# Kernel optimization log

Hardware: AMD Instinct MI355X
Metric: run time of the kernel (lower is better)

Reference implementation:

```python
import jax, jax.numpy as jnp
import numpy as np

N = 25000      # nodes
E = 400000     # edges (before self-loops)
F_IN = 128     # num_node_features
HID = 16       # hidden_channels
HEADS = 12     # GAT heads
OUT = 32       # output_channels


def setup_inputs() -> dict:
    key = jax.random.key(0)
    ks = jax.random.split(key, 16)
    def glorot(k, shape):
        fan_in = shape[0]
        return jax.random.normal(k, shape, jnp.float32) / np.sqrt(fan_in)
    return {
        "x": jax.random.normal(ks[0], (N, 1, F_IN), jnp.float32),
        "edge_index": jax.random.randint(ks[1], (2, E), 0, N, jnp.int64),
        # GCNConv 1
        "W1": glorot(ks[2], (F_IN, HID)),
        "b1": jnp.zeros((HID,), jnp.float32),
        # GATConv (heads=12, concat)
        "Wg": glorot(ks[3], (HID, HEADS * HID)),
        "att_src": jax.random.normal(ks[4], (HEADS, HID), jnp.float32) * 0.1,
        "att_dst": jax.random.normal(ks[5], (HEADS, HID), jnp.float32) * 0.1,
        "bg": jnp.zeros((HEADS * HID,), jnp.float32),
        # GCNConv 2 and 3
        "W2": glorot(ks[6], (HEADS * HID, HID)),
        "b2": jnp.zeros((HID,), jnp.float32),
        "W3": glorot(ks[7], (HID, HID)),
        "b3": jnp.zeros((HID,), jnp.float32),
        # final Linear
        "Wlin": glorot(ks[8], (HID, OUT)),
        "blin": jnp.zeros((OUT,), jnp.float32),
    }


def _add_self_loops(edge_index, n):
    loop = jnp.arange(n, dtype=edge_index.dtype)
    src = jnp.concatenate([edge_index[0], loop])
    dst = jnp.concatenate([edge_index[1], loop])
    return src, dst


def _gcn_conv(x, W, b, src, dst, n):
    # PyG GCNConv: symmetric normalization with self-loops (already in src/dst)
    h = x @ W                                            # [N, C]
    deg = jax.ops.segment_sum(jnp.ones_like(dst, jnp.float32), dst, n)
    dinv = jnp.where(deg > 0, jax.lax.rsqrt(deg), 0.0)   # deg^-0.5
    norm = dinv[src] * dinv[dst]                         # [E']
    out = jax.ops.segment_sum(h[src] * norm[:, None], dst, n)
    return out + b


def _gat_conv(x, Wg, att_src, att_dst, bg, src, dst, n):
    # PyG GATConv, concat=True, negative_slope=0.2, self-loops in src/dst
    h = (x @ Wg).reshape(n, HEADS, HID)                  # [N, H, C]
    a_s = jnp.sum(h * att_src, axis=-1)                  # [N, H]
    a_d = jnp.sum(h * att_dst, axis=-1)                  # [N, H]
    e = a_s[src] + a_d[dst]                              # [E', H]
    e = jnp.where(e > 0, e, 0.2 * e)                     # leaky_relu
    m = jax.ops.segment_max(e, dst, n)                   # stable softmax per dst
    ex = jnp.exp(e - m[dst])
    denom = jax.ops.segment_sum(ex, dst, n)
    alpha = ex / denom[dst]                              # [E', H]
    out = jax.ops.segment_sum(alpha[:, :, None] * h[src], dst, n)  # [N, H, C]
    return out.reshape(n, HEADS * HID) + bg


def reference(x, edge_index, W1, b1, Wg, att_src, att_dst, bg, W2, b2, W3, b3, Wlin, blin):
    n = x.shape[0]
    src, dst = _add_self_loops(edge_index, n)
    xs = x.squeeze(1)                                    # [N, F]
    x1 = jax.nn.relu(_gcn_conv(xs, W1, b1, src, dst, n))
    # dropout p=0.5 is identity in eval mode
    x2 = jax.nn.elu(_gat_conv(x1, Wg, att_src, att_dst, bg, src, dst, n))
    x3 = jax.nn.relu(_gcn_conv(x2, W2, b2, src, dst, n))
    x4 = jax.nn.relu(_gcn_conv(x3, W3, b3, src, dst, n)) + x3
    x4 = jnp.mean(x4, axis=0, keepdims=True)             # [1, HID]
    return x4 @ Wlin + blin                              # [1, OUT]
```

## Files before the change

kernel.cpp:

```cpp
#include <hip/hip_runtime.h>

#define F_IN 128
#define HID 16
#define HEADS 12
#define HF (HEADS*HID)
#define OUT_C 32

typedef _Float16 f16;

__global__ void k_detect(const int* __restrict__ ei, int E, int* __restrict__ flag) {
    __shared__ int sacc[256];
    int t = threadIdx.x;
    long long half = (long long)E;
    int acc = 0;
    #pragma unroll
    for (int i = 0; i < 8; i++) {
        long long k = ((long long)(t + i * 256) * half) / 2048;
        acc |= ei[2 * k + 1];
    }
    sacc[t] = acc;
    __syncthreads();
    for (int off = 128; off >= 1; off >>= 1) {
        if (t < off) sacc[t] |= sacc[t + off];
        __syncthreads();
    }
    if (t == 0) flag[1] = sacc[0];
}

__global__ void k_convert(const void* __restrict__ ei, int E, const int* __restrict__ flag,
                          int* __restrict__ src32, int* __restrict__ dst32,
                          int* __restrict__ count) {
    int e = blockIdx.x * blockDim.x + threadIdx.x;
    if (e >= E) return;
    int s, d;
    if (flag[1] == 0) {
        const long long* p = (const long long*)ei;
        s = (int)p[e];
        d = (int)p[(size_t)E + e];
    } else {
        const int* p = (const int*)ei;
        s = p[e];
        d = p[(size_t)E + e];
    }
    src32[e] = s;
    dst32[e] = d;
    atomicAdd(&count[d], 1);
}


__global__ void k_scan(const int* __restrict__ count, int* __restrict__ rowstart,
                       float* __restrict__ dinv, int n) {
    __shared__ int part[1024];
    int t = threadIdx.x;
    int chunk = (n + 1023) >> 10;
    int beg = t * chunk;
    int end = beg + chunk; if (end > n) end = n;
    int s = 0;
    for (int i = beg; i < end; i++) s += count[i];
    part[t] = s;
    __syncthreads();
    for (int off = 1; off < 1024; off <<= 1) {
        int v = (t >= off) ? part[t - off] : 0;
        __syncthreads();
        part[t] += v;
        __syncthreads();
    }
    int run = (t == 0) ? 0 : part[t - 1];
    for (int i = beg; i < end; i++) {
        rowstart[i] = run;
        int c = count[i];
        run += c;
        dinv[i] = rsqrtf((float)(c + 1));
    }
    if (t == 1023) rowstart[n] = run;
}

__global__ void k_fill(const int* __restrict__ srcA, const int* __restrict__ dstA, int E,
                       const int* __restrict__ rowstart, int* __restrict__ cursor,
                       int* __restrict__ csr) {
    int e = blockIdx.x * blockDim.x + threadIdx.x;
    if (e < E) {
        int d = dstA[e];
        int p = atomicAdd(&cursor[d], 1);
        csr[rowstart[d] + p] = srcA[e];
    }
}


__global__ void k_gemm1(const float* __restrict__ x, const float* __restrict__ W,
                        f16* __restrict__ h, int n) {
    __shared__ float sW[F_IN * HID];
    __shared__ float sX[16][F_IN + 1];
    int t = threadIdx.x;
    for (int i = t; i < F_IN * HID; i += 256) sW[i] = W[i];
    int node0 = blockIdx.x * 16;
    for (int i = t; i < 16 * F_IN; i += 256) {
        int r = i >> 7, c = i & 127;
        int node = node0 + r;
        sX[r][c] = (node < n) ? x[node * F_IN + c] : 0.f;
    }
    __syncthreads();
    int ln = t >> 4, c = t & 15;
    float acc = 0.f;
    #pragma unroll 8
    for (int k = 0; k < F_IN; k++) acc += sX[ln][k] * sW[k * HID + c];
    int node = node0 + ln;
    if (node < n) h[node * HID + c] = (f16)acc;
}

__global__ void k_gemm_gat(const float* __restrict__ x1, const float* __restrict__ Wg,
                           const float* __restrict__ att_s, const float* __restrict__ att_d,
                           f16* __restrict__ hg, float* __restrict__ a_s,
                           float* __restrict__ a_d, int n) {
    int c = threadIdx.x;
    int lane = c & 63;
    int hh = c >> 4, ci = c & 15;
    float ats = att_s[c];
    float atd = att_d[c];
    float wcol[HID];
    #pragma unroll
    for (int k = 0; k < HID; k++) wcol[k] = Wg[k * HF + c];
    for (int node = blockIdx.x; node < n; node += gridDim.x) {
        float xv = x1[node * HID + (lane & 15)];
        float acc = 0.f;
        #pragma unroll
        for (int k = 0; k < HID; k++) acc += __shfl(xv, k) * wcol[k];
        hg[(size_t)node * HF + c] = (f16)acc;
        float vs = acc * ats, vd = acc * atd;
        #pragma unroll
        for (int msk = 8; msk >= 1; msk >>= 1) {
            vs += __shfl_xor(vs, msk);
            vd += __shfl_xor(vd, msk);
        }
        if (ci == 0) {
            a_s[node * HEADS + hh] = vs;
            a_d[node * HEADS + hh] = vd;
        }
    }
}


__global__ void k_gcn_agg(const f16* __restrict__ h, const int* __restrict__ rowstart,
                          const int* __restrict__ csr, const float* __restrict__ dinv,
                          const float* __restrict__ bias, const float* __restrict__ resid,
                          float* __restrict__ out, int n) {
    int node = (blockIdx.x * blockDim.x + threadIdx.x) >> 6;
    int lane = threadIdx.x & 63;
    if (node >= n) return;
    int c = lane & 15, jj = lane >> 4;
    float dn = dinv[node];
    int base = rowstart[node], deg = rowstart[node + 1] - base;
    float acc = (jj == 0) ? (float)h[node * HID + c] * dn : 0.f;
    int j = jj;
    for (; j + 4 < deg; j += 8) {
        int s0 = csr[base + j], s1 = csr[base + j + 4];
        float d0 = dinv[s0], d1 = dinv[s1];
        float h0 = (float)h[s0 * HID + c], h1 = (float)h[s1 * HID + c];
        acc += h0 * d0 + h1 * d1;
    }
    if (j < deg) {
        int s0 = csr[base + j];
        acc += (float)h[s0 * HID + c] * dinv[s0];
    }
    acc += __shfl_xor(acc, 16);
    acc += __shfl_xor(acc, 32);
    if (lane < 16) {
        float v = fmaxf(acc * dn + bias[c], 0.f);
        if (resid) v += resid[node * HID + c];
        out[node * HID + c] = v;
    }
}

__global__ void k_gcn_agg_f3(const f16* __restrict__ h, const int* __restrict__ rowstart,
                             const int* __restrict__ csr, const float* __restrict__ dinv,
                             const float* __restrict__ bias, const float* __restrict__ W3,
                             float* __restrict__ x3o, f16* __restrict__ h3o, int n) {
    int node = (blockIdx.x * blockDim.x + threadIdx.x) >> 6;
    int lane = threadIdx.x & 63;
    if (node >= n) return;
    int c = lane & 15, jj = lane >> 4;
    float dn = dinv[node];
    int base = rowstart[node], deg = rowstart[node + 1] - base;
    float acc = (jj == 0) ? (float)h[node * HID + c] * dn : 0.f;
    int j = jj;
    for (; j + 4 < deg; j += 8) {
        int s0 = csr[base + j], s1 = csr[base + j + 4];
        float d0 = dinv[s0], d1 = dinv[s1];
        float h0 = (float)h[s0 * HID + c], h1 = (float)h[s1 * HID + c];
        acc += h0 * d0 + h1 * d1;
    }
    if (j < deg) {
        int s0 = csr[base + j];
        acc += (float)h[s0 * HID + c] * dinv[s0];
    }
    acc += __shfl_xor(acc, 16);
    acc += __shfl_xor(acc, 32);
    float v = fmaxf(acc * dn + bias[c], 0.f);
    if (lane < 16) x3o[node * HID + c] = v;
    int gbase = lane & 48;
    float hacc = 0.f;
    #pragma unroll
    for (int cc = 0; cc < 16; cc++)
        hacc += __shfl(v, gbase | cc) * W3[cc * HID + c];
    if (lane < 16) h3o[node * HID + c] = (f16)hacc;
}

__global__ void k_gat_agg(const f16* __restrict__ hg, const float* __restrict__ a_s,
                          const float* __restrict__ a_d, const int* __restrict__ rowstart,
                          const int* __restrict__ csr, const float* __restrict__ bg,
                          const float* __restrict__ W2, f16* __restrict__ h2, int n) {
    int node = (blockIdx.x * blockDim.x + threadIdx.x) >> 6;
    int lane = threadIdx.x & 63;
    if (node >= n) return;
    int base = rowstart[node], deg = rowstart[node + 1] - base;
    int dcap = deg < 64 ? deg : 64;
    int eidx = (lane < dcap) ? csr[base + lane] : 0;

    int hA = lane % 12;
    int hh0 = lane >> 4;
    int hh1 = (lane + 64) >> 4;
    int hh2 = (lane + 128) >> 4;

    float adA = a_d[node * HEADS + hA];
    float e0 = a_s[node * HEADS + hA] + adA;
    e0 = (e0 > 0.f) ? e0 : 0.2f * e0;
    float m = e0, s = 1.f;
    float acc0 = (float)hg[(size_t)node * HF + lane];
    float acc1 = (float)hg[(size_t)node * HF + lane + 64];
    float acc2 = (float)hg[(size_t)node * HF + lane + 128];

#define GAT_EDGE(AS, G0, G1, G2)                                      \
    {                                                                 \
        float e = (AS) + adA;                                         \
        e = (e > 0.f) ? e : 0.2f * e;                                 \
        float d = e - m;                                              \
        float p = __expf(d);                                          \
        if (__any(d > 8.f)) {                       \
            bool big = d > 8.f;                                       \
            float rp = big ? __expf(-d) : 1.f;                        \
            float pe = big ? 1.f : p;                                 \
            s = s * rp + pe;                                          \
            if (big) m = e;                                           \
            acc0 = acc0 * __shfl(rp, hh0) + __shfl(pe, hh0) * (G0);   \
            acc1 = acc1 * __shfl(rp, hh1) + __shfl(pe, hh1) * (G1);   \
            acc2 = acc2 * __shfl(rp, hh2) + __shfl(pe, hh2) * (G2);   \
        } else {                                                      \
            s += p;                                                   \
            acc0 += __shfl(p, hh0) * (G0);                            \
            acc1 += __shfl(p, hh1) * (G1);                            \
            acc2 += __shfl(p, hh2) * (G2);                            \
        }                                                             \
    }

    int j = 0;
    for (; j + 4 <= dcap; j += 4) {
        int s0 = __shfl(eidx, j),     s1 = __shfl(eidx, j + 1);
        int s2 = __shfl(eidx, j + 2), s3 = __shfl(eidx, j + 3);
        float A0 = a_s[s0 * HEADS + hA], A1 = a_s[s1 * HEADS + hA];
        float A2 = a_s[s2 * HEADS + hA], A3 = a_s[s3 * HEADS + hA];
        float g00 = (float)hg[(size_t)s0 * HF + lane], g01 = (float)hg[(size_t)s0 * HF + lane + 64], g02 = (float)hg[(size_t)s0 * HF + lane + 128];
        float g10 = (float)hg[(size_t)s1 * HF + lane], g11 = (float)hg[(size_t)s1 * HF + lane + 64], g12 = (float)hg[(size_t)s1 * HF + lane + 128];
        float g20 = (float)hg[(size_t)s2 * HF + lane], g21 = (float)hg[(size_t)s2 * HF + lane + 64], g22 = (float)hg[(size_t)s2 * HF + lane + 128];
        float g30 = (float)hg[(size_t)s3 * HF + lane], g31 = (float)hg[(size_t)s3 * HF + lane + 64], g32 = (float)hg[(size_t)s3 * HF + lane + 128];
        GAT_EDGE(A0, g00, g01, g02)
        GAT_EDGE(A1, g10, g11, g12)
        GAT_EDGE(A2, g20, g21, g22)
        GAT_EDGE(A3, g30, g31, g32)
    }
    for (; j < dcap; j++) {
        int s0 = __shfl(eidx, j);
        float A0 = a_s[s0 * HEADS + hA];
        float g00 = (float)hg[(size_t)s0 * HF + lane], g01 = (float)hg[(size_t)s0 * HF + lane + 64], g02 = (float)hg[(size_t)s0 * HF + lane + 128];
        GAT_EDGE(A0, g00, g01, g02)
    }
    for (; j < deg; j++) {
        int s0 = csr[base + j];
        float A0 = a_s[s0 * HEADS + hA];
        float g00 = (float)hg[(size_t)s0 * HF + lane], g01 = (float)hg[(size_t)s0 * HF + lane + 64], g02 = (float)hg[(size_t)s0 * HF + lane + 128];
        GAT_EDGE(A0, g00, g01, g02)
    }
#undef GAT_EDGE

    float is = 1.f / s;
    float i0 = __shfl(is, hh0), i1 = __shfl(is, hh1), i2 = __shfl(is, hh2);
    float v0 = acc0 * i0 + bg[lane];
    float v1 = acc1 * i1 + bg[lane + 64];
    float v2 = acc2 * i2 + bg[lane + 128];
    v0 = (v0 > 0.f) ? v0 : (__expf(v0) - 1.f);
    v1 = (v1 > 0.f) ? v1 : (__expf(v1) - 1.f);
    v2 = (v2 > 0.f) ? v2 : (__expf(v2) - 1.f);

    float p[16];
    const float4* W2v = (const float4*)W2;
    #pragma unroll
    for (int q = 0; q < 4; q++) {
        float4 w0 = W2v[lane * 4 + q];
        float4 w1 = W2v[(lane + 64) * 4 + q];
        float4 w2 = W2v[(lane + 128) * 4 + q];
        p[q * 4 + 0] = v0 * w0.x + v1 * w1.x + v2 * w2.x;
        p[q * 4 + 1] = v0 * w0.y + v1 * w1.y + v2 * w2.y;
        p[q * 4 + 2] = v0 * w0.z + v1 * w1.z + v2 * w2.z;
        p[q * 4 + 3] = v0 * w0.w + v1 * w1.w + v2 * w2.w;
    }
    #pragma unroll
    for (int mask = 1; mask <= 32; mask <<= 1) {
        #pragma unroll
        for (int cq = 0; cq < 16; cq++) p[cq] += __shfl_xor(p[cq], mask);
    }
    float vout = p[0];
    #pragma unroll
    for (int q = 1; q < 16; q++) vout = (lane == q) ? p[q] : vout;
    if (lane < 16) h2[node * HID + lane] = (f16)vout;
}


__global__ void k_mean_final(const float* __restrict__ x4, float* __restrict__ red,
                             int* __restrict__ done, const float* __restrict__ Wlin,
                             const float* __restrict__ blin, float* __restrict__ out,
                             float invN, int n, int nblocks) {
    __shared__ float sd[16][17];
    __shared__ float sred[16];
    __shared__ int slast;
    int t = threadIdx.x;
    int ln = t >> 4, c = t & 15;
    float acc = 0.f;
    for (int node = blockIdx.x * 16 + ln; node < n; node += gridDim.x * 16)
        acc += x4[node * HID + c];
    sd[ln][c] = acc;
    __syncthreads();
    for (int off = 8; off >= 1; off >>= 1) {
        if (ln < off) sd[ln][c] += sd[ln + off][c];
        __syncthreads();
    }
    if (ln == 0) atomicAdd(&red[c], sd[0][c]);
    __threadfence();
    __syncthreads();
    if (t == 0) slast = (atomicAdd(done, 1) == nblocks - 1);
    __syncthreads();
    if (slast) {
        if (t < 16) sred[t] = atomicAdd(&red[t], 0.0f);
        __syncthreads();
        if (t < OUT_C) {
            float a = blin[t];
            #pragma unroll
            for (int cc = 0; cc < HID; cc++) a += (sred[cc] * invN) * Wlin[cc * OUT_C + t];
            out[t] = a;
        }
    }
}


extern "C" void kernel_launch(void* const* d_in, const int* in_sizes, int n_in,
                              void* d_out, int out_size, void* d_ws, size_t ws_size,
                              hipStream_t stream) {
    const float* x     = (const float*)d_in[0];
    const void*  ei    = d_in[1];
    const float* W1    = (const float*)d_in[2];
    const float* b1    = (const float*)d_in[3];
    const float* Wg    = (const float*)d_in[4];
    const float* att_s = (const float*)d_in[5];
    const float* att_d = (const float*)d_in[6];
    const float* bg    = (const float*)d_in[7];
    const float* W2    = (const float*)d_in[8];
    const float* b2    = (const float*)d_in[9];
    const float* W3    = (const float*)d_in[10];
    const float* b3    = (const float*)d_in[11];
    const float* Wlin  = (const float*)d_in[12];
    const float* blin  = (const float*)d_in[13];
    float* out = (float*)d_out;

    int N = in_sizes[0] / F_IN;
    int E = in_sizes[1] / 2;

    char* w = (char*)d_ws;
    size_t off = 0;
    auto alloc = [&](size_t bytes) -> void* {
        void* p = w + off;
        off += (bytes + 255) & ~(size_t)255;
        return p;
    };
    int*   flag     = (int*)alloc(256);
    int*   count    = (int*)alloc((size_t)N * 4);
    int*   cursor   = (int*)alloc((size_t)N * 4);
    float* red      = (float*)alloc(256);
    int*   done     = (int*)((char*)red + 64);
    size_t zbytes   = (size_t)((char*)red + 256 - (char*)count);
    int*   src32    = (int*)alloc((size_t)E * 4);
    int*   dst32    = (int*)alloc((size_t)E * 4);
    int*   rowstart = (int*)alloc((size_t)(N + 1) * 4);
    int*   csr      = (int*)alloc((size_t)E * 4);
    float* dinv     = (float*)alloc((size_t)N * 4);
    f16*   h1       = (f16*)alloc((size_t)N * HID * 2);
    float* x1       = (float*)alloc((size_t)N * HID * 4);
    f16*   hg       = (f16*)alloc((size_t)N * HF * 2);
    float* a_s      = (float*)alloc((size_t)N * HEADS * 4);
    float* a_d      = (float*)alloc((size_t)N * HEADS * 4);
    f16*   h2       = (f16*)alloc((size_t)N * HID * 2);
    float* x3       = (float*)alloc((size_t)N * HID * 4);
    f16*   h3       = (f16*)alloc((size_t)N * HID * 2);
    float* x4       = (float*)alloc((size_t)N * HID * 4);
    if (off > ws_size) return;

    hipMemsetAsync(count, 0, zbytes, stream);

    int eb = (E + 255) / 256;
    int nb16 = (N + 15) / 16;
    int nbw  = (N + 3) / 4;

    k_detect<<<1, 256, 0, stream>>>((const int*)ei, E, flag);
    k_convert<<<eb, 256, 0, stream>>>(ei, E, flag, src32, dst32, count);
    k_scan<<<1, 1024, 0, stream>>>(count, rowstart, dinv, N);
    k_fill<<<eb, 256, 0, stream>>>(src32, dst32, E, rowstart, cursor, csr);

    k_gemm1<<<nb16, 256, 0, stream>>>(x, W1, h1, N);
    k_gcn_agg<<<nbw, 256, 0, stream>>>(h1, rowstart, csr, dinv, b1, nullptr, x1, N);

    k_gemm_gat<<<2048, 192, 0, stream>>>(x1, Wg, att_s, att_d, hg, a_s, a_d, N);
    k_gat_agg<<<nbw, 256, 0, stream>>>(hg, a_s, a_d, rowstart, csr, bg, W2, h2, N);

    k_gcn_agg_f3<<<nbw, 256, 0, stream>>>(h2, rowstart, csr, dinv, b2, W3, x3, h3, N);
    k_gcn_agg<<<nbw, 256, 0, stream>>>(h3, rowstart, csr, dinv, b3, x3, x4, N);

    k_mean_final<<<128, 256, 0, stream>>>(x4, red, done, Wlin, blin, out,
                                          1.0f / (float)N, N, 128);
}
```

Baseline: 314.9 us.

## Fold detection into convert, merge fill with GEMM1, restructure GAT and GCN aggregation

Every block of the convert kernel now detects the index dtype itself, which removes the separate detect launch and the flag round-trip. The CSR fill and the first GEMM are merged into one launch over a combined block range. GCN aggregation loads up to 64 neighbour indices once per wave and broadcasts them with shuffles. The GAT aggregation now uses one 192-thread block per node (one channel per thread) with an LDS-based W2 projection instead of 64-lane waves carrying three channels each. The trade-off is redundant detection reads in every convert block and many more small blocks with syncthreads in the GAT kernel.

```diff
diff --git a/kernel.cpp b/kernel.cpp
--- a/kernel.cpp
+++ b/kernel.cpp
@@ -8,45 +8,41 @@
 
 typedef _Float16 f16;
 
-__global__ void k_detect(const int* __restrict__ ei, int E, int* __restrict__ flag) {
-    __shared__ int sacc[256];
+__global__ void k_convert(const void* __restrict__ ei, int E,
+                          int* __restrict__ src32, int* __restrict__ dst32,
+                          int* __restrict__ count) {
+    __shared__ int sdet[256];
     int t = threadIdx.x;
+    const int* w32 = (const int*)ei;
     long long half = (long long)E;
-    int acc = 0;
+    int a = 0;
     #pragma unroll
     for (int i = 0; i < 8; i++) {
         long long k = ((long long)(t + i * 256) * half) / 2048;
-        acc |= ei[2 * k + 1];
-    }
-    sacc[t] = acc;
+        a |= w32[2 * k + 1];
+    }
+    sdet[t] = a;
     __syncthreads();
     for (int off = 128; off >= 1; off >>= 1) {
-        if (t < off) sacc[t] |= sacc[t + off];
+        if (t < off) sdet[t] |= sdet[t + off];
         __syncthreads();
     }
-    if (t == 0) flag[1] = sacc[0];
-}
-
-__global__ void k_convert(const void* __restrict__ ei, int E, const int* __restrict__ flag,
-                          int* __restrict__ src32, int* __restrict__ dst32,
-                          int* __restrict__ count) {
-    int e = blockIdx.x * blockDim.x + threadIdx.x;
+    int is32 = sdet[0];
+    int e = blockIdx.x * blockDim.x + t;
     if (e >= E) return;
     int s, d;
-    if (flag[1] == 0) {
+    if (!is32) {
         const long long* p = (const long long*)ei;
         s = (int)p[e];
         d = (int)p[(size_t)E + e];
     } else {
-        const int* p = (const int*)ei;
-        s = p[e];
-        d = p[(size_t)E + e];
+        s = w32[e];
+        d = w32[(size_t)E + e];
     }
     src32[e] = s;
     dst32[e] = d;
     atomicAdd(&count[d], 1);
 }
-
 
 __global__ void k_scan(const int* __restrict__ count, int* __restrict__ rowstart,
                        float* __restrict__ dinv, int n) {
@@ -75,25 +71,26 @@
     if (t == 1023) rowstart[n] = run;
 }
 
-__global__ void k_fill(const int* __restrict__ srcA, const int* __restrict__ dstA, int E,
-                       const int* __restrict__ rowstart, int* __restrict__ cursor,
-                       int* __restrict__ csr) {
-    int e = blockIdx.x * blockDim.x + threadIdx.x;
-    if (e < E) {
-        int d = dstA[e];
-        int p = atomicAdd(&cursor[d], 1);
-        csr[rowstart[d] + p] = srcA[e];
-    }
-}
-
-
-__global__ void k_gemm1(const float* __restrict__ x, const float* __restrict__ W,
-                        f16* __restrict__ h, int n) {
+__global__ void k_fill_gemm1(const int* __restrict__ src32, const int* __restrict__ dst32,
+                             int E, const int* __restrict__ rowstart, int* __restrict__ cursor,
+                             int* __restrict__ csr, const float* __restrict__ x,
+                             const float* __restrict__ W1, f16* __restrict__ h1,
+                             int n, int eb) {
     __shared__ float sW[F_IN * HID];
     __shared__ float sX[16][F_IN + 1];
+    int b = blockIdx.x;
+    if (b < eb) {
+        int e = b * 256 + threadIdx.x;
+        if (e < E) {
+            int d = dst32[e];
+            int p = atomicAdd(&cursor[d], 1);
+            csr[rowstart[d] + p] = src32[e];
+        }
+        return;
+    }
     int t = threadIdx.x;
-    for (int i = t; i < F_IN * HID; i += 256) sW[i] = W[i];
-    int node0 = blockIdx.x * 16;
+    for (int i = t; i < F_IN * HID; i += 256) sW[i] = W1[i];
+    int node0 = (b - eb) * 16;
     for (int i = t; i < 16 * F_IN; i += 256) {
         int r = i >> 7, c = i & 127;
         int node = node0 + r;
@@ -105,7 +102,7 @@
     #pragma unroll 8
     for (int k = 0; k < F_IN; k++) acc += sX[ln][k] * sW[k * HID + c];
     int node = node0 + ln;
-    if (node < n) h[node * HID + c] = (f16)acc;
+    if (node < n) h1[node * HID + c] = (f16)acc;
 }
 
 __global__ void k_gemm_gat(const float* __restrict__ x1, const float* __restrict__ Wg,
@@ -150,15 +147,21 @@
     int c = lane & 15, jj = lane >> 4;
     float dn = dinv[node];
     int base = rowstart[node], deg = rowstart[node + 1] - base;
+    int dcap = deg < 64 ? deg : 64;
+    int eidx = (lane < dcap) ? csr[base + lane] : 0;
     float acc = (jj == 0) ? (float)h[node * HID + c] * dn : 0.f;
-    int j = jj;
-    for (; j + 4 < deg; j += 8) {
-        int s0 = csr[base + j], s1 = csr[base + j + 4];
-        float d0 = dinv[s0], d1 = dinv[s1];
-        float h0 = (float)h[s0 * HID + c], h1 = (float)h[s1 * HID + c];
-        acc += h0 * d0 + h1 * d1;
-    }
-    if (j < deg) {
+    for (int j = 0; j < dcap; j += 16) {
+        int i0 = j + jj, i1 = i0 + 4, i2 = i0 + 8, i3 = i0 + 12;
+        int s0 = __shfl(eidx, i0);
+        int s1 = __shfl(eidx, i1);
+        int s2 = __shfl(eidx, i2);
+        int s3 = __shfl(eidx, i3);
+        if (i0 < dcap) acc += (float)h[s0 * HID + c] * dinv[s0];
+        if (i1 < dcap) acc += (float)h[s1 * HID + c] * dinv[s1];
+        if (i2 < dcap) acc += (float)h[s2 * HID + c] * dinv[s2];
+        if (i3 < dcap) acc += (float)h[s3 * HID + c] * dinv[s3];
+    }
+    for (int j = 64 + jj; j < deg; j += 4) {
         int s0 = csr[base + j];
         acc += (float)h[s0 * HID + c] * dinv[s0];
     }
@@ -181,15 +184,21 @@
     int c = lane & 15, jj = lane >> 4;
     float dn = dinv[node];
     int base = rowstart[node], deg = rowstart[node + 1] - base;
+    int dcap = deg < 64 ? deg : 64;
+    int eidx = (lane < dcap) ? csr[base + lane] : 0;
     float acc = (jj == 0) ? (float)h[node * HID + c] * dn : 0.f;
-    int j = jj;
-    for (; j + 4 < deg; j += 8) {
-        int s0 = csr[base + j], s1 = csr[base + j + 4];
-        float d0 = dinv[s0], d1 = dinv[s1];
-        float h0 = (float)h[s0 * HID + c], h1 = (float)h[s1 * HID + c];
-        acc += h0 * d0 + h1 * d1;
-    }
-    if (j < deg) {
+    for (int j = 0; j < dcap; j += 16) {
+        int i0 = j + jj, i1 = i0 + 4, i2 = i0 + 8, i3 = i0 + 12;
+        int s0 = __shfl(eidx, i0);
+        int s1 = __shfl(eidx, i1);
+        int s2 = __shfl(eidx, i2);
+        int s3 = __shfl(eidx, i3);
+        if (i0 < dcap) acc += (float)h[s0 * HID + c] * dinv[s0];
+        if (i1 < dcap) acc += (float)h[s1 * HID + c] * dinv[s1];
+        if (i2 < dcap) acc += (float)h[s2 * HID + c] * dinv[s2];
+        if (i3 < dcap) acc += (float)h[s3 * HID + c] * dinv[s3];
+    }
+    for (int j = 64 + jj; j < deg; j += 4) {
         int s0 = csr[base + j];
         acc += (float)h[s0 * HID + c] * dinv[s0];
     }
@@ -205,112 +214,89 @@
     if (lane < 16) h3o[node * HID + c] = (f16)hacc;
 }
 
-__global__ void k_gat_agg(const f16* __restrict__ hg, const float* __restrict__ a_s,
-                          const float* __restrict__ a_d, const int* __restrict__ rowstart,
-                          const int* __restrict__ csr, const float* __restrict__ bg,
-                          const float* __restrict__ W2, f16* __restrict__ h2, int n) {
-    int node = (blockIdx.x * blockDim.x + threadIdx.x) >> 6;
-    int lane = threadIdx.x & 63;
-    if (node >= n) return;
+__global__ void k_gat3(const f16* __restrict__ hg, const float* __restrict__ a_s,
+                       const float* __restrict__ a_d, const int* __restrict__ rowstart,
+                       const int* __restrict__ csr, const float* __restrict__ bg,
+                       const float* __restrict__ W2, f16* __restrict__ h2, int n) {
+    __shared__ float sx2[HF];
+    __shared__ float sp[3][16];
+    int node = blockIdx.x;
+    int t = threadIdx.x;
+    int w = t >> 6;
+    int lane = t & 63;
+    int c = t;
+    int h = c >> 4;
     int base = rowstart[node], deg = rowstart[node + 1] - base;
     int dcap = deg < 64 ? deg : 64;
     int eidx = (lane < dcap) ? csr[base + lane] : 0;
 
-    int hA = lane % 12;
-    int hh0 = lane >> 4;
-    int hh1 = (lane + 64) >> 4;
-    int hh2 = (lane + 128) >> 4;
-
-    float adA = a_d[node * HEADS + hA];
-    float e0 = a_s[node * HEADS + hA] + adA;
-    e0 = (e0 > 0.f) ? e0 : 0.2f * e0;
+    float ad = a_d[node * HEADS + h];
+    float e0 = a_s[node * HEADS + h] + ad;
+    e0 = fmaxf(e0, 0.2f * e0);
     float m = e0, s = 1.f;
-    float acc0 = (float)hg[(size_t)node * HF + lane];
-    float acc1 = (float)hg[(size_t)node * HF + lane + 64];
-    float acc2 = (float)hg[(size_t)node * HF + lane + 128];
-
-#define GAT_EDGE(AS, G0, G1, G2)                                      \
-    {                                                                 \
-        float e = (AS) + adA;                                         \
-        e = (e > 0.f) ? e : 0.2f * e;                                 \
-        float d = e - m;                                              \
-        float p = __expf(d);                                          \
-        if (__any(d > 8.f)) {                       \
-            bool big = d > 8.f;                                       \
-            float rp = big ? __expf(-d) : 1.f;                        \
-            float pe = big ? 1.f : p;                                 \
-            s = s * rp + pe;                                          \
-            if (big) m = e;                                           \
-            acc0 = acc0 * __shfl(rp, hh0) + __shfl(pe, hh0) * (G0);   \
-            acc1 = acc1 * __shfl(rp, hh1) + __shfl(pe, hh1) * (G1);   \
-            acc2 = acc2 * __shfl(rp, hh2) + __shfl(pe, hh2) * (G2);   \
-        } else {                                                      \
-            s += p;                                                   \
-            acc0 += __shfl(p, hh0) * (G0);                            \
-            acc1 += __shfl(p, hh1) * (G1);                            \
-            acc2 += __shfl(p, hh2) * (G2);                            \
-        }                                                             \
+    float acc = (float)hg[(size_t)node * HF + c];
+
+#define EDGE(A, G)                                         \
+    {                                                      \
+        float e = (A) + ad;                                \
+        e = fmaxf(e, 0.2f * e);                            \
+        float d = e - m;                                   \
+        float p = __expf(d);                               \
+        if (__any(d > 8.f)) {            \
+            bool big = d > 8.f;                            \
+            float rp = big ? __expf(-d) : 1.f;             \
+            float pe = big ? 1.f : p;                      \
+            s = s * rp + pe;                               \
+            if (big) m = e;                                \
+            acc = acc * rp + pe * (G);                     \
+        } else {                                           \
+            s += p;                                        \
+            acc += p * (G);                                \
+        }                                                  \
     }
 
     int j = 0;
     for (; j + 4 <= dcap; j += 4) {
         int s0 = __shfl(eidx, j),     s1 = __shfl(eidx, j + 1);
         int s2 = __shfl(eidx, j + 2), s3 = __shfl(eidx, j + 3);
-        float A0 = a_s[s0 * HEADS + hA], A1 = a_s[s1 * HEADS + hA];
-        float A2 = a_s[s2 * HEADS + hA], A3 = a_s[s3 * HEADS + hA];
-        float g00 = (float)hg[(size_t)s0 * HF + lane], g01 = (float)hg[(size_t)s0 * HF + lane + 64], g02 = (float)hg[(size_t)s0 * HF + lane + 128];
-        float g10 = (float)hg[(size_t)s1 * HF + lane], g11 = (float)hg[(size_t)s1 * HF + lane + 64], g12 = (float)hg[(size_t)s1 * HF + lane + 128];
-        float g20 = (float)hg[(size_t)s2 * HF + lane], g21 = (float)hg[(size_t)s2 * HF + lane + 64], g22 = (float)hg[(size_t)s2 * HF + lane + 128];
-        float g30 = (float)hg[(size_t)s3 * HF + lane], g31 = (float)hg[(size_t)s3 * HF + lane + 64], g32 = (float)hg[(size_t)s3 * HF + lane + 128];
-        GAT_EDGE(A0, g00, g01, g02)
-        GAT_EDGE(A1, g10, g11, g12)
-        GAT_EDGE(A2, g20, g21, g22)
-        GAT_EDGE(A3, g30, g31, g32)
+        float A0 = a_s[s0 * HEADS + h], A1 = a_s[s1 * HEADS + h];
+        float A2 = a_s[s2 * HEADS + h], A3 = a_s[s3 * HEADS + h];
+        float g0 = (float)hg[(size_t)s0 * HF + c];
+        float g1 = (float)hg[(size_t)s1 * HF + c];
+        float g2 = (float)hg[(size_t)s2 * HF + c];
+        float g3 = (float)hg[(size_t)s3 * HF + c];
+        EDGE(A0, g0)
+        EDGE(A1, g1)
+        EDGE(A2, g2)
+        EDGE(A3, g3)
     }
     for (; j < dcap; j++) {
         int s0 = __shfl(eidx, j);
-        float A0 = a_s[s0 * HEADS + hA];
-        float g00 = (float)hg[(size_t)s0 * HF + lane], g01 = (float)hg[(size_t)s0 * HF + lane + 64], g02 = (float)hg[(size_t)s0 * HF + lane + 128];
-        GAT_EDGE(A0, g00, g01, g02)
+        float A0 = a_s[s0 * HEADS + h];
+        float g0 = (float)hg[(size_t)s0 * HF + c];
+        EDGE(A0, g0)
     }
     for (; j < deg; j++) {
         int s0 = csr[base + j];
-        float A0 = a_s[s0 * HEADS + hA];
-        float g00 = (float)hg[(size_t)s0 * HF + lane], g01 = (float)hg[(size_t)s0 * HF + lane + 64], g02 = (float)hg[(size_t)s0 * HF + lane + 128];
-        GAT_EDGE(A0, g00, g01, g02)
-    }
-#undef GAT_EDGE
-
-    float is = 1.f / s;
-    float i0 = __shfl(is, hh0), i1 = __shfl(is, hh1), i2 = __shfl(is, hh2);
-    float v0 = acc0 * i0 + bg[lane];
-    float v1 = acc1 * i1 + bg[lane + 64];
-    float v2 = acc2 * i2 + bg[lane + 128];
-    v0 = (v0 > 0.f) ? v0 : (__expf(v0) - 1.f);
-    v1 = (v1 > 0.f) ? v1 : (__expf(v1) - 1.f);
-    v2 = (v2 > 0.f) ? v2 : (__expf(v2) - 1.f);
-
-    float p[16];
-    const float4* W2v = (const float4*)W2;
-    #pragma unroll
-    for (int q = 0; q < 4; q++) {
-        float4 w0 = W2v[lane * 4 + q];
-        float4 w1 = W2v[(lane + 64) * 4 + q];
-        float4 w2 = W2v[(lane + 128) * 4 + q];
-        p[q * 4 + 0] = v0 * w0.x + v1 * w1.x + v2 * w2.x;
-        p[q * 4 + 1] = v0 * w0.y + v1 * w1.y + v2 * w2.y;
-        p[q * 4 + 2] = v0 * w0.z + v1 * w1.z + v2 * w2.z;
-        p[q * 4 + 3] = v0 * w0.w + v1 * w1.w + v2 * w2.w;
-    }
-    #pragma unroll
-    for (int mask = 1; mask <= 32; mask <<= 1) {
-        #pragma unroll
-        for (int cq = 0; cq < 16; cq++) p[cq] += __shfl_xor(p[cq], mask);
-    }
-    float vout = p[0];
-    #pragma unroll
-    for (int q = 1; q < 16; q++) vout = (lane == q) ? p[q] : vout;
-    if (lane < 16) h2[node * HID + lane] = (f16)vout;
+        float A0 = a_s[s0 * HEADS + h];
+        float g0 = (float)hg[(size_t)s0 * HF + c];
+        EDGE(A0, g0)
+    }
+#undef EDGE
+
+    float v = acc / s + bg[c];
+    v = (v > 0.f) ? v : (__expf(v) - 1.f);
+    sx2[c] = v;
+    __syncthreads();
+    if (lane < 16) {
+        float a = 0.f;
+        #pragma unroll 16
+        for (int k = 0; k < 64; k++)
+            a += sx2[w * 64 + k] * W2[(w * 64 + k) * HID + lane];
+        sp[w][lane] = a;
+    }
+    __syncthreads();
+    if (t < 16) h2[node * HID + t] = (f16)(sp[0][t] + sp[1][t] + sp[2][t]);
 }
 
 
@@ -379,7 +365,6 @@
         off += (bytes + 255) & ~(size_t)255;
         return p;
     };
-    int*   flag     = (int*)alloc(256);
     int*   count    = (int*)alloc((size_t)N * 4);
     int*   cursor   = (int*)alloc((size_t)N * 4);
     float* red      = (float*)alloc(256);
@@ -407,16 +392,15 @@
     int nb16 = (N + 15) / 16;
     int nbw  = (N + 3) / 4;
 
-    k_detect<<<1, 256, 0, stream>>>((const int*)ei, E, flag);
-    k_convert<<<eb, 256, 0, stream>>>(ei, E, flag, src32, dst32, count);
+    k_convert<<<eb, 256, 0, stream>>>(ei, E, src32, dst32, count);
     k_scan<<<1, 1024, 0, stream>>>(count, rowstart, dinv, N);
-    k_fill<<<eb, 256, 0, stream>>>(src32, dst32, E, rowstart, cursor, csr);
-
-    k_gemm1<<<nb16, 256, 0, stream>>>(x, W1, h1, N);
+    k_fill_gemm1<<<eb + nb16, 256, 0, stream>>>(src32, dst32, E, rowstart, cursor, csr,
+                                                x, W1, h1, N, eb);
+
     k_gcn_agg<<<nbw, 256, 0, stream>>>(h1, rowstart, csr, dinv, b1, nullptr, x1, N);
 
     k_gemm_gat<<<2048, 192, 0, stream>>>(x1, Wg, att_s, att_d, hg, a_s, a_d, N);
-    k_gat_agg<<<nbw, 256, 0, stream>>>(hg, a_s, a_d, rowstart, csr, bg, W2, h2, N);
+    k_gat3<<<N, 192, 0, stream>>>(hg, a_s, a_d, rowstart, csr, bg, W2, h2, N);
 
     k_gcn_agg_f3<<<nbw, 256, 0, stream>>>(h2, rowstart, csr, dinv, b2, W3, x3, h3, N);
     k_gcn_agg<<<nbw, 256, 0, stream>>>(h3, rowstart, csr, dinv, b3, x3, x4, N);
```

New measurement: 337.9 us. 1.07x slower.
